# Kernel optimization log

Measured on AMD Instinct MI355X. Metric: run time of the kernel, lower is better.

The kernel has to match this reference:

```python
import jax, jax.numpy as jnp
import numpy as np

# Dims: T time steps (PoissonEncoder seq_length=50), batch B, input N_IN, hidden H, labels L
T, B, N_IN, H, L = 50, 1024, 784, 256, 10
DT = 0.001            # norse default dt
TAU_SYN_INV = 100.0   # 1/0.01
TAU_MEM_INV = 50.0    # 1/0.02
V_LEAK, V_TH, V_RESET = 0.0, 0.5, 0.0
ALPHA = 100.0         # SuperSpike surrogate slope

@jax.custom_vjp
def superspike(x):
    # Heaviside forward, SuperSpike surrogate backward (norse 'super' method)
    return (x > 0).astype(x.dtype)

def _ss_fwd(x):
    return superspike(x), x

def _ss_bwd(x, g):
    return (g / (ALPHA * jnp.abs(x) + 1.0) ** 2,)

superspike.defvjp(_ss_fwd, _ss_bwd)

def setup_inputs() -> dict:
    key = jax.random.key(0)
    ks = jax.random.split(key, 5)
    # Poisson-encoded spike train, time-major [T, B, N_IN]
    x = (jax.random.uniform(ks[0], (T, B, N_IN)) < 0.3).astype(jnp.float32)
    Wi = jax.random.normal(ks[1], (H, N_IN), dtype=jnp.float32) / np.float32(np.sqrt(N_IN))
    Wr = jax.random.normal(ks[2], (H, H), dtype=jnp.float32) / np.float32(np.sqrt(H))
    Wout = jax.random.normal(ks[3], (L, H), dtype=jnp.float32) / np.float32(np.sqrt(H))
    bout = jnp.zeros((L,), dtype=jnp.float32)
    return {"x": x, "Wi": Wi, "Wr": Wr, "Wout": Wout, "bout": bout}

def reference(x, Wi, Wr, Wout, bout):
    Tw, Bb, _ = x.shape
    Hh = Wi.shape[0]
    Ll = Wout.shape[0]
    z0 = jnp.zeros((Bb, Hh), x.dtype)
    acc0 = jnp.zeros((Bb, Ll), x.dtype)

    def step(carry, x_t):
        z, v, i, acc = carry
        # LIF dynamics (norse lif_step)
        v_dec = v + DT * TAU_MEM_INV * ((V_LEAK - v) + i)   # voltage integration
        i_dec = i * (1.0 - DT * TAU_SYN_INV)                # synaptic current decay
        z_new = superspike(v_dec - V_TH)                    # spike
        v_new = (1.0 - z_new) * v_dec + z_new * V_RESET     # reset
        i_new = i_dec + x_t @ Wi.T + z @ Wr.T               # input + recurrent drive
        # per-step readout accumulation
        acc = acc + z_new @ Wout.T + bout
        return (z_new, v_new, i_new, acc), None

    (_, _, _, acc), _ = jax.lax.scan(step, (z0, z0, z0, acc0), x)
    return acc / Tw  # outputs.float() / time_window (is_test=False path)
```

## Files before the change

### kernel.cpp

```cpp
#include <hip/hip_runtime.h>
#include <cstdint>
#include <cstddef>

#define T_STEPS 50
#define B_SZ    1024
#define N_INP   784
#define H_SZ    256
#define L_SZ    10
#define M_TOT   (T_STEPS * B_SZ)
#define NK0     26
#define NSLICE  5

typedef int v4i  __attribute__((ext_vector_type(4)));
typedef int v16i __attribute__((ext_vector_type(16)));

__global__ __launch_bounds__(256) void transpose_wr(const float* __restrict__ Wr,
                                                    float* __restrict__ WrTz) {
    __shared__ float tile[32][33];
    int bx = blockIdx.x * 32, by = blockIdx.y * 32;
    int tx = threadIdx.x % 32, ty = threadIdx.x / 32;
    #pragma unroll
    for (int j = 0; j < 32; j += 8)
        tile[ty + j][tx] = Wr[(size_t)(by + ty + j) * H_SZ + bx + tx];
    if (blockIdx.x == 0 && blockIdx.y == 0)
        WrTz[(size_t)256 * H_SZ + threadIdx.x] = 0.0f;
    __syncthreads();
    #pragma unroll
    for (int j = 0; j < 32; j += 8)
        WrTz[(size_t)(bx + ty + j) * H_SZ + by + tx] = tile[tx][ty + j];
}

__global__ __launch_bounds__(128) void prep_packed(const float* __restrict__ Wi,
                                                   uint8_t* __restrict__ SBp) {
    const int nt   = blockIdx.x;
    const int k0   = blockIdx.y * 2 + (threadIdx.x >> 6);
    const int lane = threadIdx.x & 63;
    const int h    = nt * 32 + (lane & 31);
    const int g    = k0 * 2 + (lane >> 5);

    int wd[NSLICE][4] = {};
    #pragma unroll
    for (int u = 0; u < 16; ++u) {
        double wv = 0.0;
        if (g < 49) wv = (double)Wi[(size_t)h * N_INP + g * 16 + u];
        double r = rint(wv * 0x1p40);
        #pragma unroll
        for (int j = 0; j < NSLICE - 1; ++j) {
            double q  = floor((r + 128.0) * 0.00390625);
            double dj = r - 256.0 * q;
            wd[j][u >> 2] |= ((int)dj & 0xFF) << ((u & 3) * 8);
            r = q;
        }
        wd[NSLICE - 1][u >> 2] |= ((int)r & 0xFF) << ((u & 3) * 8);
    }
    uint8_t* base = SBp + ((size_t)(nt * NK0 + k0) * NSLICE) * 1024 + lane * 16;
    #pragma unroll
    for (int j = 0; j < NSLICE; ++j)
        *(v4i*)(base + (size_t)j * 1024) = (v4i){wd[j][0], wd[j][1], wd[j][2], wd[j][3]};
}

__global__ __launch_bounds__(256) void pack_x(const float* __restrict__ X,
                                              uint8_t* __restrict__ Ap) {
    const int mt  = blockIdx.x;
    const int tid = threadIdx.x;
    #pragma unroll
    for (int i = 0; i < 7; ++i) {
        int s = tid + i * 256;
        if (s < NK0 * 64) {
            int k0 = s >> 6, lane = s & 63;
            int m = mt * 32 + (lane & 31);
            int g = k0 * 2 + (lane >> 5);
            unsigned int bw[4] = {0u, 0u, 0u, 0u};
            if (g < 49) {
                const float* src = X + (size_t)m * N_INP + g * 16;
                #pragma unroll
                for (int q = 0; q < 4; ++q) {
                    float4 f = *(const float4*)(src + q * 4);
                    bw[q] = (f.x != 0.f ? 1u : 0u) | (f.y != 0.f ? 0x100u : 0u)
                          | (f.z != 0.f ? 0x10000u : 0u) | (f.w != 0.f ? 0x1000000u : 0u);
                }
            }
            *(v4i*)(Ap + ((size_t)(mt * NK0 + k0)) * 1024 + lane * 16) =
                (v4i){(int)bw[0], (int)bw[1], (int)bw[2], (int)bw[3]};
        }
    }
}

typedef __attribute__((address_space(1))) uint32_t glds_g;
typedef __attribute__((address_space(3))) uint32_t glds_l;

#define STAGE_B(dstbuf, srcp, NI)                                               \
    {                                                                           \
        _Pragma("unroll")                                                       \
        for (int j_ = 0; j_ < (NI); ++j_) {                                     \
            int s_ = j_ * 256 + tid;                                            \
            __builtin_amdgcn_global_load_lds(                                   \
                (glds_g*)((srcp) + (size_t)s_ * 16),                            \
                (glds_l*)((dstbuf) + (size_t)s_ * 16), 16, 0, 0);               \
        }                                                                       \
    }

#define MFMA_STAGE(CB, A0, A1, NK)                                              \
    _Pragma("unroll")                                                           \
    for (int dk = 0; dk < (NK); ++dk) {                                         \
        _Pragma("unroll")                                                       \
        for (int j = 0; j < NSLICE; ++j) {                                      \
            v4i b = *(const v4i*)(Bs[CB] + (dk * NSLICE + j) * 1024 + lane * 16); \
            acc0[j] = __builtin_amdgcn_mfma_i32_32x32x32_i8(A0[dk], b, acc0[j], 0, 0, 0); \
            acc1[j] = __builtin_amdgcn_mfma_i32_32x32x32_i8(A1[dk], b, acc1[j], 0, 0, 0); \
        }                                                                       \
    }

__global__ __launch_bounds__(256) void gemm_i8s(const uint8_t* __restrict__ Ap,
                                                const uint8_t* __restrict__ SBp,
                                                double* __restrict__ cur) {
    __shared__ __align__(16) uint8_t Bs[2][4 * NSLICE * 1024];

    const int tid   = threadIdx.x;
    const int wave  = tid >> 6;
    const int lane  = tid & 63;
    const int ghalf = lane >> 5;
    const int nt    = blockIdx.y;
    const int mt0   = (blockIdx.x * 4 + wave) * 2;
    const int mt1   = mt0 + 1;

    const uint8_t* ap0 = Ap + (size_t)mt0 * NK0 * 1024 + lane * 16;
    const uint8_t* ap1 = Ap + (size_t)mt1 * NK0 * 1024 + lane * 16;
    const uint8_t* bbase = SBp + ((size_t)nt * NK0 * NSLICE) * 1024;

    v4i a0[4], a1[4], n0[4], n1[4];

    STAGE_B(Bs[0], bbase, 5);
    #pragma unroll
    for (int dk = 0; dk < 4; ++dk) {
        a0[dk] = *(const v4i*)(ap0 + (size_t)dk * 1024);
        a1[dk] = *(const v4i*)(ap1 + (size_t)dk * 1024);
    }
    __syncthreads();

    v16i acc0[NSLICE] = {};
    v16i acc1[NSLICE] = {};

    for (int s = 0; s < 6; ++s) {
        const int cb = s & 1;
        if (s < 5) {
            STAGE_B(Bs[cb ^ 1], bbase + (size_t)(s + 1) * 20480, 5);
            #pragma unroll
            for (int dk = 0; dk < 4; ++dk) {
                n0[dk] = *(const v4i*)(ap0 + (size_t)((s + 1) * 4 + dk) * 1024);
                n1[dk] = *(const v4i*)(ap1 + (size_t)((s + 1) * 4 + dk) * 1024);
            }
        } else {
            STAGE_B(Bs[cb ^ 1], bbase + (size_t)6 * 20480, 3);
            #pragma unroll
            for (int dk = 0; dk < 2; ++dk) {
                n0[dk] = *(const v4i*)(ap0 + (size_t)(24 + dk) * 1024);
                n1[dk] = *(const v4i*)(ap1 + (size_t)(24 + dk) * 1024);
            }
        }
        MFMA_STAGE(cb, a0, a1, 4);
        __syncthreads();
        #pragma unroll
        for (int dk = 0; dk < 4; ++dk) { a0[dk] = n0[dk]; a1[dk] = n1[dk]; }
    }
    MFMA_STAGE(0, a0, a1, 2);

    const int h = nt * 32 + (lane & 31);
    #pragma unroll
    for (int r = 0; r < 16; ++r) {
        int mloc = (r & 3) + 8 * (r >> 2) + 4 * ghalf;
        double s0 = (double)acc0[4][r];
        s0 = s0 * 256.0 + (double)acc0[3][r];
        s0 = s0 * 256.0 + (double)acc0[2][r];
        s0 = s0 * 256.0 + (double)acc0[1][r];
        s0 = s0 * 256.0 + (double)acc0[0][r];
        cur[(size_t)(mt0 * 32 + mloc) * H_SZ + h] = s0 * 0x1p-40;
        double s1 = (double)acc1[4][r];
        s1 = s1 * 256.0 + (double)acc1[3][r];
        s1 = s1 * 256.0 + (double)acc1[2][r];
        s1 = s1 * 256.0 + (double)acc1[1][r];
        s1 = s1 * 256.0 + (double)acc1[0][r];
        cur[(size_t)(mt1 * 32 + mloc) * H_SZ + h] = s1 * 0x1p-40;
    }
}

__global__ __launch_bounds__(256) void snn_scan(const double* __restrict__ cur,
                                                const float* __restrict__ WrTz,
                                                const float* __restrict__ Wout,
                                                const float* __restrict__ bout,
                                                float* __restrict__ out) {
    const int b    = blockIdx.x;
    const int h    = threadIdx.x;
    const int wv   = h >> 6;
    const int lane = h & 63;

    __shared__ unsigned long long zmS[2][4];
    __shared__ __align__(16) int listS[2][4][264];
    __shared__ float cntS[H_SZ];

    double v = 0.0, syn = 0.0;
    int cnt = 0;
    int nn[2] = {0, 0};

    const double* curb = cur + (size_t)b * H_SZ + h;
    const char*   wrb  = (const char*)WrTz;
    const uint32_t hoff = (uint32_t)(h * 4);
    double inp_c = curb[0];

    for (int t = 0; t < T_STEPS; ++t) {
        const int p = t & 1;
        const int q = p ^ 1;
        int tn = (t < T_STEPS - 1) ? t + 1 : t;
        double inp_n = curb[(size_t)tn * B_SZ * H_SZ];

        double v_dec = v + 0.05 * ((0.0 - v) + syn);
        double i_dec = 0.9 * syn;
        bool   z_new = v_dec > 0.5;
        v = z_new ? 0.0 : v_dec;
        cnt += z_new ? 1 : 0;

        double r0 = 0.0, r1 = 0.0, r2 = 0.0, r3 = 0.0;
        const int* lp = listS[p][wv];
        const int  n  = nn[p];
        for (int j = 0; j < n; j += 8) {
            v4i w0 = *(const v4i*)(lp + j);
            v4i w1 = *(const v4i*)(lp + j + 4);
            float f0 = *(const float*)(wrb + ((uint32_t)w0.x + hoff));
            float f1 = *(const float*)(wrb + ((uint32_t)w0.y + hoff));
            float f2 = *(const float*)(wrb + ((uint32_t)w0.z + hoff));
            float f3 = *(const float*)(wrb + ((uint32_t)w0.w + hoff));
            float f4 = *(const float*)(wrb + ((uint32_t)w1.x + hoff));
            float f5 = *(const float*)(wrb + ((uint32_t)w1.y + hoff));
            float f6 = *(const float*)(wrb + ((uint32_t)w1.z + hoff));
            float f7 = *(const float*)(wrb + ((uint32_t)w1.w + hoff));
            r0 += (double)f0 + (double)f1;
            r1 += (double)f2 + (double)f3;
            r2 += (double)f4 + (double)f5;
            r3 += (double)f6 + (double)f7;
        }

        unsigned long long bal = __ballot((int)z_new);
        if (lane == 0) zmS[q][wv] = bal;
        __syncthreads();

        {
            unsigned long long m0 = zmS[q][0], m1 = zmS[q][1],
                               m2 = zmS[q][2], m3 = zmS[q][3];
            int c0 = __popcll(m0), c1 = __popcll(m1),
                c2 = __popcll(m2), c3 = __popcll(m3);
            const int wi = lane >> 4;
            unsigned long long word = zmS[q][wi];
            int basew = (wi > 0 ? c0 : 0) + (wi > 1 ? c1 : 0) + (wi > 2 ? c2 : 0);
            int* lw = listS[q][wv];
            const int hb = 4 * lane;
            #pragma unroll
            for (int u = 0; u < 4; ++u) {
                int bit = (hb + u) & 63;
                bool act = (word >> bit) & 1ull;
                int  pos = __popcll(word & ((1ull << bit) - 1ull));
                if (act) lw[basew + pos] = (hb + u) << 10;
            }
            int tot = c0 + c1 + c2 + c3;
            if (lane < 8) lw[tot + lane] = 256 << 10;
            nn[q] = tot;
        }

        syn = (i_dec + inp_c) + ((r0 + r1) + (r2 + r3));
        inp_c = inp_n;
    }

    cntS[h] = (float)cnt;
    __syncthreads();
    if (h < L_SZ) {
        double s = 0.0;
        for (int k = 0; k < H_SZ; ++k)
            s += (double)cntS[k] * (double)Wout[(size_t)h * H_SZ + k];
        s += (double)T_STEPS * (double)bout[h];
        out[(size_t)b * L_SZ + h] = (float)(s / (double)T_STEPS);
    }
}

extern "C" void kernel_launch(void* const* d_in, const int* in_sizes, int n_in,
                              void* d_out, int out_size, void* d_ws, size_t ws_size,
                              hipStream_t stream) {
    const float* x    = (const float*)d_in[0];
    const float* Wi   = (const float*)d_in[1];
    const float* Wr   = (const float*)d_in[2];
    const float* Wout = (const float*)d_in[3];
    const float* bout = (const float*)d_in[4];
    float* out = (float*)d_out;

    char* ws = (char*)d_ws;
    double*  cur  = (double*)(ws);
    float*   WrTz = (float*)(ws + 104857600);
    uint8_t* SBp  = (uint8_t*)(ws + 105121792);
    uint8_t* Ap   = (uint8_t*)(ws + 106186752);

    hipLaunchKernelGGL(transpose_wr, dim3(8, 8), dim3(256), 0, stream, Wr, WrTz);
    hipLaunchKernelGGL(prep_packed, dim3(8, 13), dim3(128), 0, stream, Wi, SBp);
    hipLaunchKernelGGL(pack_x, dim3(M_TOT / 32), dim3(256), 0, stream, x, Ap);
    hipLaunchKernelGGL(gemm_i8s, dim3(M_TOT / 256, 8), dim3(256), 0, stream, Ap, SBp, cur);
    hipLaunchKernelGGL(snn_scan, dim3(B_SZ), dim3(256), 0, stream,
                       cur, WrTz, Wout, bout, out);
}
```

Baseline: 383.4 us.

## Map one batch row per wavefront and cache Wr rows in LDS

The scan kernel now processes four batch rows per block, one per wavefront. Each lane owns four hidden units, which removes the per-step __syncthreads and lets the spike list be built with wave ballots alone. The first 144 rows of the transposed recurrent weights are staged in shared memory, and the remaining rows are read from global memory with float4 loads using software-pipelined prefetch. This aims to cut block-level synchronisation and global gather latency, at the cost of a large LDS footprint (about 150 KB), which limits the kernel to one block per CU, and a quarter as many blocks.

```diff
diff --git a/kernel.cpp b/kernel.cpp
--- a/kernel.cpp
+++ b/kernel.cpp
@@ -184,99 +184,194 @@
     }
 }
 
-__global__ __launch_bounds__(256) void snn_scan(const double* __restrict__ cur,
-                                                const float* __restrict__ WrTz,
-                                                const float* __restrict__ Wout,
-                                                const float* __restrict__ bout,
-                                                float* __restrict__ out) {
-    const int b    = blockIdx.x;
-    const int h    = threadIdx.x;
-    const int wv   = h >> 6;
-    const int lane = h & 63;
-
-    __shared__ unsigned long long zmS[2][4];
-    __shared__ __align__(16) int listS[2][4][264];
-    __shared__ float cntS[H_SZ];
-
-    double v = 0.0, syn = 0.0;
-    int cnt = 0;
-    int nn[2] = {0, 0};
-
-    const double* curb = cur + (size_t)b * H_SZ + h;
-    const char*   wrb  = (const char*)WrTz;
-    const uint32_t hoff = (uint32_t)(h * 4);
-    double inp_c = curb[0];
+#define ACC8(A0,A1,A2,A3,A4,A5,A6,A7)                          \
+    r0 += (double)A0.x + (double)A1.x;                         \
+    r1 += (double)A0.y + (double)A1.y;                         \
+    r2 += (double)A0.z + (double)A1.z;                         \
+    r3 += (double)A0.w + (double)A1.w;                         \
+    r0 += (double)A2.x + (double)A3.x;                         \
+    r1 += (double)A2.y + (double)A3.y;                         \
+    r2 += (double)A2.z + (double)A3.z;                         \
+    r3 += (double)A2.w + (double)A3.w;                         \
+    r0 += (double)A4.x + (double)A5.x;                         \
+    r1 += (double)A4.y + (double)A5.y;                         \
+    r2 += (double)A4.z + (double)A5.z;                         \
+    r3 += (double)A4.w + (double)A5.w;                         \
+    r0 += (double)A6.x + (double)A7.x;                         \
+    r1 += (double)A6.y + (double)A7.y;                         \
+    r2 += (double)A6.z + (double)A7.z;                         \
+    r3 += (double)A6.w + (double)A7.w;
+
+__global__ __launch_bounds__(256, 1) void snn_scan(const double* __restrict__ cur,
+                                                   const float* __restrict__ WrTz,
+                                                   const float* __restrict__ Wout,
+                                                   const float* __restrict__ bout,
+                                                   float* __restrict__ out) {
+    const int tid  = threadIdx.x;
+    const int wv   = tid >> 6;
+    const int lane = tid & 63;
+    const int b    = blockIdx.x * 4 + wv;
+
+    __shared__ __align__(16) float WrL[145 * 256];
+    __shared__ __align__(16) int   listLo[4][160];
+    __shared__ __align__(16) int   listHi[4][136];
+    __shared__ float cntW[4][256];
+
+    for (int s = tid; s < 145 * 64; s += 256) {
+        float4 val = (s < 144 * 64) ? ((const float4*)WrTz)[s]
+                                    : make_float4(0.f, 0.f, 0.f, 0.f);
+        ((float4*)WrL)[s] = val;
+    }
+    __syncthreads();
+
+    double vv[4]   = {0.0, 0.0, 0.0, 0.0};
+    double syn[4]  = {0.0, 0.0, 0.0, 0.0};
+    double inpc[4];
+    int    cnt[4]  = {0, 0, 0, 0};
+    unsigned long long mOld[4] = {0ull, 0ull, 0ull, 0ull};
+
+    const double* curb = cur + (size_t)b * H_SZ + 4 * lane;
+    {
+        double2 a0 = *(const double2*)(curb);
+        double2 a1 = *(const double2*)(curb + 2);
+        inpc[0] = a0.x; inpc[1] = a0.y; inpc[2] = a1.x; inpc[3] = a1.y;
+    }
+
+    const char*    wrb    = (const char*)WrTz;
+    const int      lane4  = lane * 4;
+    const uint32_t lane16 = (uint32_t)(lane * 16);
+    const unsigned long long lm = (1ull << lane) - 1ull;
+    const int rb = 4 * lane;
+
+    int* lo = listLo[wv];
+    int* hi = listHi[wv];
 
     for (int t = 0; t < T_STEPS; ++t) {
-        const int p = t & 1;
-        const int q = p ^ 1;
+        double idc[4]; bool z[4];
+        #pragma unroll
+        for (int j = 0; j < 4; ++j) {
+            double vd = vv[j] + 0.05 * ((0.0 - vv[j]) + syn[j]);
+            idc[j] = 0.9 * syn[j];
+            z[j]   = vd > 0.5;
+            vv[j]  = z[j] ? 0.0 : vd;
+            cnt[j] += z[j] ? 1 : 0;
+        }
+        unsigned long long mNew[4];
+        #pragma unroll
+        for (int j = 0; j < 4; ++j) mNew[j] = __ballot((int)z[j]);
+
         int tn = (t < T_STEPS - 1) ? t + 1 : t;
-        double inp_n = curb[(size_t)tn * B_SZ * H_SZ];
-
-        double v_dec = v + 0.05 * ((0.0 - v) + syn);
-        double i_dec = 0.9 * syn;
-        bool   z_new = v_dec > 0.5;
-        v = z_new ? 0.0 : v_dec;
-        cnt += z_new ? 1 : 0;
+        double2 ina = *(const double2*)(curb + (size_t)tn * (B_SZ * H_SZ));
+        double2 inb = *(const double2*)(curb + (size_t)tn * (B_SZ * H_SZ) + 2);
+
+        const unsigned long long LOWM = (1ull << 36) - 1ull;
+        int pl[4], bj[4], cL[4], cA[4];
+        #pragma unroll
+        for (int j = 0; j < 4; ++j) {
+            pl[j] = __popcll(mOld[j] & lm);
+            bj[j] = (int)((mOld[j] >> lane) & 1ull);
+            cL[j] = __popcll(mOld[j] & LOWM);
+            cA[j] = __popcll(mOld[j]);
+        }
+        const int below = pl[0] + pl[1] + pl[2] + pl[3];
+        const int nLo   = cL[0] + cL[1] + cL[2] + cL[3];
+        const int nHi   = (cA[0] + cA[1] + cA[2] + cA[3]) - nLo;
+        if (lane < 36) {
+            int p = below;
+            if (bj[0]) lo[p] = (rb + 0) << 8;  p += bj[0];
+            if (bj[1]) lo[p] = (rb + 1) << 8;  p += bj[1];
+            if (bj[2]) lo[p] = (rb + 2) << 8;  p += bj[2];
+            if (bj[3]) lo[p] = (rb + 3) << 8;
+        } else {
+            int p = below - nLo;
+            if (bj[0]) hi[p] = (rb + 0) << 10; p += bj[0];
+            if (bj[1]) hi[p] = (rb + 1) << 10; p += bj[1];
+            if (bj[2]) hi[p] = (rb + 2) << 10; p += bj[2];
+            if (bj[3]) hi[p] = (rb + 3) << 10;
+        }
+        if (lane < 16) lo[nLo + lane] = 144 << 8;
+        if (lane < 24) hi[nHi + lane] = 256 << 10;
 
         double r0 = 0.0, r1 = 0.0, r2 = 0.0, r3 = 0.0;
-        const int* lp = listS[p][wv];
-        const int  n  = nn[p];
-        for (int j = 0; j < n; j += 8) {
-            v4i w0 = *(const v4i*)(lp + j);
-            v4i w1 = *(const v4i*)(lp + j + 4);
-            float f0 = *(const float*)(wrb + ((uint32_t)w0.x + hoff));
-            float f1 = *(const float*)(wrb + ((uint32_t)w0.y + hoff));
-            float f2 = *(const float*)(wrb + ((uint32_t)w0.z + hoff));
-            float f3 = *(const float*)(wrb + ((uint32_t)w0.w + hoff));
-            float f4 = *(const float*)(wrb + ((uint32_t)w1.x + hoff));
-            float f5 = *(const float*)(wrb + ((uint32_t)w1.y + hoff));
-            float f6 = *(const float*)(wrb + ((uint32_t)w1.z + hoff));
-            float f7 = *(const float*)(wrb + ((uint32_t)w1.w + hoff));
-            r0 += (double)f0 + (double)f1;
-            r1 += (double)f2 + (double)f3;
-            r2 += (double)f4 + (double)f5;
-            r3 += (double)f6 + (double)f7;
-        }
-
-        unsigned long long bal = __ballot((int)z_new);
-        if (lane == 0) zmS[q][wv] = bal;
-        __syncthreads();
-
         {
-            unsigned long long m0 = zmS[q][0], m1 = zmS[q][1],
-                               m2 = zmS[q][2], m3 = zmS[q][3];
-            int c0 = __popcll(m0), c1 = __popcll(m1),
-                c2 = __popcll(m2), c3 = __popcll(m3);
-            const int wi = lane >> 4;
-            unsigned long long word = zmS[q][wi];
-            int basew = (wi > 0 ? c0 : 0) + (wi > 1 ? c1 : 0) + (wi > 2 ? c2 : 0);
-            int* lw = listS[q][wv];
-            const int hb = 4 * lane;
-            #pragma unroll
-            for (int u = 0; u < 4; ++u) {
-                int bit = (hb + u) & 63;
-                bool act = (word >> bit) & 1ull;
-                int  pos = __popcll(word & ((1ull << bit) - 1ull));
-                if (act) lw[basew + pos] = (hb + u) << 10;
+            v4i h0 = *(const v4i*)(hi + 0),  h1 = *(const v4i*)(hi + 4);
+            float4 GA0 = *(const float4*)(wrb + ((uint32_t)h0.x + lane16));
+            float4 GA1 = *(const float4*)(wrb + ((uint32_t)h0.y + lane16));
+            float4 GA2 = *(const float4*)(wrb + ((uint32_t)h0.z + lane16));
+            float4 GA3 = *(const float4*)(wrb + ((uint32_t)h0.w + lane16));
+            float4 GA4 = *(const float4*)(wrb + ((uint32_t)h1.x + lane16));
+            float4 GA5 = *(const float4*)(wrb + ((uint32_t)h1.y + lane16));
+            float4 GA6 = *(const float4*)(wrb + ((uint32_t)h1.z + lane16));
+            float4 GA7 = *(const float4*)(wrb + ((uint32_t)h1.w + lane16));
+            v4i h2 = *(const v4i*)(hi + 8),  h3 = *(const v4i*)(hi + 12);
+            float4 GB0 = *(const float4*)(wrb + ((uint32_t)h2.x + lane16));
+            float4 GB1 = *(const float4*)(wrb + ((uint32_t)h2.y + lane16));
+            float4 GB2 = *(const float4*)(wrb + ((uint32_t)h2.z + lane16));
+            float4 GB3 = *(const float4*)(wrb + ((uint32_t)h2.w + lane16));
+            float4 GB4 = *(const float4*)(wrb + ((uint32_t)h3.x + lane16));
+            float4 GB5 = *(const float4*)(wrb + ((uint32_t)h3.y + lane16));
+            float4 GB6 = *(const float4*)(wrb + ((uint32_t)h3.z + lane16));
+            float4 GB7 = *(const float4*)(wrb + ((uint32_t)h3.w + lane16));
+
+            v4i l0 = *(const v4i*)(lo + 0), l1 = *(const v4i*)(lo + 4);
+            float4 LA0 = *(const float4*)(WrL + (l0.x + lane4));
+            float4 LA1 = *(const float4*)(WrL + (l0.y + lane4));
+            float4 LA2 = *(const float4*)(WrL + (l0.z + lane4));
+            float4 LA3 = *(const float4*)(WrL + (l0.w + lane4));
+            float4 LA4 = *(const float4*)(WrL + (l1.x + lane4));
+            float4 LA5 = *(const float4*)(WrL + (l1.y + lane4));
+            float4 LA6 = *(const float4*)(WrL + (l1.z + lane4));
+            float4 LA7 = *(const float4*)(WrL + (l1.w + lane4));
+            for (int j = 0; j < nLo; j += 8) {
+                v4i u0 = *(const v4i*)(lo + j + 8), u1 = *(const v4i*)(lo + j + 12);
+                float4 LB0 = *(const float4*)(WrL + (u0.x + lane4));
+                float4 LB1 = *(const float4*)(WrL + (u0.y + lane4));
+                float4 LB2 = *(const float4*)(WrL + (u0.z + lane4));
+                float4 LB3 = *(const float4*)(WrL + (u0.w + lane4));
+                float4 LB4 = *(const float4*)(WrL + (u1.x + lane4));
+                float4 LB5 = *(const float4*)(WrL + (u1.y + lane4));
+                float4 LB6 = *(const float4*)(WrL + (u1.z + lane4));
+                float4 LB7 = *(const float4*)(WrL + (u1.w + lane4));
+                ACC8(LA0, LA1, LA2, LA3, LA4, LA5, LA6, LA7)
+                LA0 = LB0; LA1 = LB1; LA2 = LB2; LA3 = LB3;
+                LA4 = LB4; LA5 = LB5; LA6 = LB6; LA7 = LB7;
             }
-            int tot = c0 + c1 + c2 + c3;
-            if (lane < 8) lw[tot + lane] = 256 << 10;
-            nn[q] = tot;
-        }
-
-        syn = (i_dec + inp_c) + ((r0 + r1) + (r2 + r3));
-        inp_c = inp_n;
-    }
-
-    cntS[h] = (float)cnt;
-    __syncthreads();
-    if (h < L_SZ) {
+
+            for (int j = 0; j < nHi; j += 8) {
+                v4i u0 = *(const v4i*)(hi + j + 16), u1 = *(const v4i*)(hi + j + 20);
+                float4 GC0 = *(const float4*)(wrb + ((uint32_t)u0.x + lane16));
+                float4 GC1 = *(const float4*)(wrb + ((uint32_t)u0.y + lane16));
+                float4 GC2 = *(const float4*)(wrb + ((uint32_t)u0.z + lane16));
+                float4 GC3 = *(const float4*)(wrb + ((uint32_t)u0.w + lane16));
+                float4 GC4 = *(const float4*)(wrb + ((uint32_t)u1.x + lane16));
+                float4 GC5 = *(const float4*)(wrb + ((uint32_t)u1.y + lane16));
+                float4 GC6 = *(const float4*)(wrb + ((uint32_t)u1.z + lane16));
+                float4 GC7 = *(const float4*)(wrb + ((uint32_t)u1.w + lane16));
+                ACC8(GA0, GA1, GA2, GA3, GA4, GA5, GA6, GA7)
+                GA0 = GB0; GA1 = GB1; GA2 = GB2; GA3 = GB3;
+                GA4 = GB4; GA5 = GB5; GA6 = GB6; GA7 = GB7;
+                GB0 = GC0; GB1 = GC1; GB2 = GC2; GB3 = GC3;
+                GB4 = GC4; GB5 = GC5; GB6 = GC6; GB7 = GC7;
+            }
+        }
+
+        syn[0] = (idc[0] + inpc[0]) + r0;
+        syn[1] = (idc[1] + inpc[1]) + r1;
+        syn[2] = (idc[2] + inpc[2]) + r2;
+        syn[3] = (idc[3] + inpc[3]) + r3;
+        inpc[0] = ina.x; inpc[1] = ina.y; inpc[2] = inb.x; inpc[3] = inb.y;
+        #pragma unroll
+        for (int j = 0; j < 4; ++j) mOld[j] = mNew[j];
+    }
+
+    #pragma unroll
+    for (int j = 0; j < 4; ++j) cntW[wv][rb + j] = (float)cnt[j];
+    if (lane < L_SZ) {
         double s = 0.0;
         for (int k = 0; k < H_SZ; ++k)
-            s += (double)cntS[k] * (double)Wout[(size_t)h * H_SZ + k];
-        s += (double)T_STEPS * (double)bout[h];
-        out[(size_t)b * L_SZ + h] = (float)(s / (double)T_STEPS);
+            s += (double)cntW[wv][k] * (double)Wout[(size_t)lane * H_SZ + k];
+        s += (double)T_STEPS * (double)bout[lane];
+        out[(size_t)b * L_SZ + lane] = (float)(s / (double)T_STEPS);
     }
 }
 
@@ -300,6 +395,6 @@
     hipLaunchKernelGGL(prep_packed, dim3(8, 13), dim3(128), 0, stream, Wi, SBp);
     hipLaunchKernelGGL(pack_x, dim3(M_TOT / 32), dim3(256), 0, stream, x, Ap);
     hipLaunchKernelGGL(gemm_i8s, dim3(M_TOT / 256, 8), dim3(256), 0, stream, Ap, SBp, cur);
-    hipLaunchKernelGGL(snn_scan, dim3(B_SZ), dim3(256), 0, stream,
+    hipLaunchKernelGGL(snn_scan, dim3(B_SZ / 4), dim3(256), 0, stream,
                        cur, WrTz, Wout, bout, out);
 }
```

Measured after the change: 407.3 us. +6.2%, slower.
